# Performance work log

Measured on AMD Instinct MI355X. Metric: run time of the kernel, lower is better.

Reference implementation:

```python
import jax, jax.numpy as jnp
import numpy as np

NOISE_STD = 0.1

def setup_inputs() -> dict:
    key = jax.random.key(0)
    k1, k2, k3, k4 = jax.random.split(key, 4)
    B, S, D, E, NS = 4, 4096, 2048, 64, 10
    x = jax.random.normal(k1, (B, S, D), dtype=jnp.float32)
    W = jax.random.normal(k2, (E, D), dtype=jnp.float32) * (1.0 / np.sqrt(D))
    scale_condition = jax.random.normal(k3, (NS, 1, 1), dtype=jnp.float32)
    noise = jax.random.normal(k4, (B, S, E), dtype=jnp.float32)
    return {"x": x, "W": W, "scale_condition": scale_condition, "noise": noise, "scale_idx": 3}

def reference(x, W, scale_condition, noise, scale_idx):
    TOP_K = 2
    E = W.shape[0]
    # scale modulation: scale_condition[scale_idx] has shape [1,1], broadcasts over [B,S,D]
    scale_factor = scale_condition[scale_idx]
    router_input = x * (1.0 + scale_factor * 0.1)
    # small GEMM: [B,S,D] x [D,E] -> [B,S,E]
    router_logits = jnp.einsum('bsd,ed->bse', router_input, W)
    router_logits = router_logits + noise * NOISE_STD
    routing_probs = jax.nn.softmax(router_logits, axis=-1)
    routing_weights, selected_experts = jax.lax.top_k(routing_probs, TOP_K)
    routing_weights = routing_weights / jnp.sum(routing_weights, axis=-1, keepdims=True)
    # scatter top-k normalized weights into dense [B,S,E] dispatch tensor
    dispatch_tensor = jnp.sum(
        jax.nn.one_hot(selected_experts, E, dtype=routing_weights.dtype)
        * routing_weights[..., None],
        axis=-2,
    )
    return dispatch_tensor, routing_probs, selected_experts
```

## Files before the change

kernel.cpp:

```cpp
#include <hip/hip_runtime.h>
#include <math.h>

#define D        2048
#define E        64
#define NROWS    16384
#define NSLICE   4
#define KSLICE   (D / NSLICE)
#define BK       32
#define TILES    (KSLICE / BK)
#define BM       32
#define XSTR     36
#define OSTR     68
#define PARTIAL_BYTES ((size_t)NSLICE * NROWS * E * 4)

__global__ __launch_bounds__(64)
void gemm_ks(const float* __restrict__ x,
             const float* __restrict__ W,
             const float* __restrict__ scond,
             const int* __restrict__ sidx,
             float* __restrict__ partial)
{
    __shared__ float smem[BM * XSTR + BK * E];
    float* xs = smem;
    float* ws = smem + BM * XSTR;

    const int l = threadIdx.x;
    const int slice   = blockIdx.x & (NSLICE - 1);
    const int rowBase = (blockIdx.x >> 2) * BM;
    const int kBase   = slice * KSLICE;

    const float factor = 1.0f + 0.1f * scond[sidx[0]];

    const int sxr = l >> 1;
    const int sxh = (l & 1) << 4;

    const int rg = l & 7;
    const int eg = l >> 3;

    float acc[4][8];
#pragma unroll
    for (int i = 0; i < 4; ++i)
#pragma unroll
        for (int j = 0; j < 8; ++j) acc[i][j] = 0.f;

    const float* xg = x + (size_t)rowBase * D + kBase;
    const float* wg = W + (size_t)l * D + kBase;

    float4 xb[4], wb[8];
#pragma unroll
    for (int j = 0; j < 4; ++j)
        xb[j] = *(const float4*)(xg + sxr * D + sxh + (j << 2));
#pragma unroll
    for (int j = 0; j < 8; ++j)
        wb[j] = *(const float4*)(wg + (j << 2));

    for (int t = 0; t < TILES; ++t) {
#pragma unroll
        for (int j = 0; j < 4; ++j) {
            float4 v = xb[j];
            v.x *= factor; v.y *= factor; v.z *= factor; v.w *= factor;
            *(float4*)&xs[sxr * XSTR + sxh + (j << 2)] = v;
        }
#pragma unroll
        for (int j = 0; j < 8; ++j) {
            const int k4 = j << 2;
            ws[(k4 + 0) * E + l] = wb[j].x;
            ws[(k4 + 1) * E + l] = wb[j].y;
            ws[(k4 + 2) * E + l] = wb[j].z;
            ws[(k4 + 3) * E + l] = wb[j].w;
        }

        if (t + 1 < TILES) {
            const int k0 = (t + 1) * BK;
#pragma unroll
            for (int j = 0; j < 4; ++j)
                xb[j] = *(const float4*)(xg + sxr * D + k0 + sxh + (j << 2));
#pragma unroll
            for (int j = 0; j < 8; ++j)
                wb[j] = *(const float4*)(wg + k0 + (j << 2));
        }

#pragma unroll
        for (int kc = 0; kc < 8; ++kc) {
            float4 xv[4];
#pragma unroll
            for (int i = 0; i < 4; ++i)
                xv[i] = *(const float4*)&xs[(rg + 8 * i) * XSTR + (kc << 2)];
            float4 wv[8];
#pragma unroll
            for (int k = 0; k < 4; ++k) {
                wv[2 * k]     = *(const float4*)&ws[((kc << 2) + k) * E + (eg << 3)];
                wv[2 * k + 1] = *(const float4*)&ws[((kc << 2) + k) * E + (eg << 3) + 4];
            }
#pragma unroll
            for (int k = 0; k < 4; ++k) {
#pragma unroll
                for (int i = 0; i < 4; ++i) {
                    const float xk = ((const float*)&xv[i])[k];
                    acc[i][0] += xk * wv[2 * k].x;
                    acc[i][1] += xk * wv[2 * k].y;
                    acc[i][2] += xk * wv[2 * k].z;
                    acc[i][3] += xk * wv[2 * k].w;
                    acc[i][4] += xk * wv[2 * k + 1].x;
                    acc[i][5] += xk * wv[2 * k + 1].y;
                    acc[i][6] += xk * wv[2 * k + 1].z;
                    acc[i][7] += xk * wv[2 * k + 1].w;
                }
            }
        }
    }

#pragma unroll
    for (int i = 0; i < 4; ++i) {
        float4 a0, a1;
        a0.x = acc[i][0]; a0.y = acc[i][1]; a0.z = acc[i][2]; a0.w = acc[i][3];
        a1.x = acc[i][4]; a1.y = acc[i][5]; a1.z = acc[i][6]; a1.w = acc[i][7];
        *(float4*)&smem[(rg + 8 * i) * OSTR + (eg << 3)]     = a0;
        *(float4*)&smem[(rg + 8 * i) * OSTR + (eg << 3) + 4] = a1;
    }
    float* pbase = partial + (size_t)slice * NROWS * E + (size_t)rowBase * E;
#pragma unroll
    for (int j = 0; j < 8; ++j) {
        const int p   = (j << 6) + l;
        const int row = p >> 4;
        const int c4  = p & 15;
        const float4 vv = *(const float4*)&smem[row * OSTR + (c4 << 2)];
        *(float4*)(pbase + ((size_t)p << 2)) = vv;
    }
}

__global__ __launch_bounds__(256)
void reduce_topk(const float* __restrict__ partial,
                 const float* __restrict__ noise,
                 float* __restrict__ dispatch,
                 float* __restrict__ probs,
                 float* __restrict__ sel)
{
    const int lane = threadIdx.x & 63;
    const int wave = threadIdx.x >> 6;
    const int row  = blockIdx.x * 4 + wave;

    float v = 0.f;
#pragma unroll
    for (int s = 0; s < NSLICE; ++s)
        v += partial[(size_t)s * NROWS * E + (size_t)row * E + lane];
    v += 0.1f * noise[(size_t)row * E + lane];

    float m = v;
#pragma unroll
    for (int off = 32; off > 0; off >>= 1)
        m = fmaxf(m, __shfl_xor(m, off, 64));
    const float p = expf(v - m);
    float s = p;
#pragma unroll
    for (int off = 32; off > 0; off >>= 1)
        s += __shfl_xor(s, off, 64);
    const float prob = p / s;
    probs[(size_t)row * E + lane] = prob;

    float bv = prob; int bi = lane;
#pragma unroll
    for (int off = 32; off > 0; off >>= 1) {
        const float ov = __shfl_xor(bv, off, 64);
        const int   oi = __shfl_xor(bi, off, 64);
        if (ov > bv || (ov == bv && oi < bi)) { bv = ov; bi = oi; }
    }
    float cv = (lane == bi) ? -INFINITY : prob;
    int ci = lane;
#pragma unroll
    for (int off = 32; off > 0; off >>= 1) {
        const float ov = __shfl_xor(cv, off, 64);
        const int   oi = __shfl_xor(ci, off, 64);
        if (ov > cv || (ov == cv && oi < ci)) { cv = ov; ci = oi; }
    }

    const float sum2 = bv + cv;
    float dval = 0.f;
    if (lane == bi) dval = bv / sum2;
    if (lane == ci) dval = cv / sum2;
    dispatch[(size_t)row * E + lane] = dval;

    if (lane == 0) {
        float2 sv; sv.x = (float)bi; sv.y = (float)ci;
        *(float2*)(sel + (size_t)row * 2) = sv;
    }
}

__global__ __launch_bounds__(256)
void gemm_r2(const float* __restrict__ x, const float* __restrict__ W,
             const float* __restrict__ scond, const float* __restrict__ noise,
             const int* __restrict__ sidx, float* __restrict__ logits_out)
{
    __shared__ float4 xsb[32][17];
    __shared__ float4 wsh[64][16];
    const int tid = threadIdx.x;
    const int rowBase = blockIdx.x * 32;
    const float factor = 1.0f + 0.1f * scond[sidx[0]];
    const int xk = tid & 15, xr = tid >> 4, we = tid & 63, wk = tid >> 6;
    const int eg = tid & 15, rg = tid >> 4, e0 = eg << 2;
    float acc[2][4];
#pragma unroll
    for (int i = 0; i < 2; ++i)
#pragma unroll
        for (int j = 0; j < 4; ++j) acc[i][j] = 0.f;
    const float* xg = x + (size_t)rowBase * D;
    float4 xb[2], wb[4];
#pragma unroll
    for (int i = 0; i < 2; ++i)
        xb[i] = *(const float4*)(xg + (xr + 16 * i) * D + (xk << 2));
#pragma unroll
    for (int j = 0; j < 4; ++j)
        wb[j] = *(const float4*)(W + we * D + (wk << 4) + (j << 2));
    for (int t = 0; t < 32; ++t) {
#pragma unroll
        for (int i = 0; i < 2; ++i) {
            float4 v = xb[i];
            v.x *= factor; v.y *= factor; v.z *= factor; v.w *= factor;
            xsb[xr + 16 * i][xk] = v;
        }
        float* wsf = (float*)wsh;
#pragma unroll
        for (int j = 0; j < 4; ++j) {
            const int kk = (wk << 4) + (j << 2);
            wsf[(kk + 0) * E + we] = wb[j].x;
            wsf[(kk + 1) * E + we] = wb[j].y;
            wsf[(kk + 2) * E + we] = wb[j].z;
            wsf[(kk + 3) * E + we] = wb[j].w;
        }
        __syncthreads();
        if (t + 1 < 32) {
            const int k0 = (t + 1) * 64;
#pragma unroll
            for (int i = 0; i < 2; ++i)
                xb[i] = *(const float4*)(xg + (xr + 16 * i) * D + k0 + (xk << 2));
#pragma unroll
            for (int j = 0; j < 4; ++j)
                wb[j] = *(const float4*)(W + we * D + k0 + (wk << 4) + (j << 2));
        }
#pragma unroll
        for (int kg = 0; kg < 16; ++kg) {
            float4 xv[2], wv[4];
#pragma unroll
            for (int i = 0; i < 2; ++i) xv[i] = xsb[rg + 16 * i][kg];
#pragma unroll
            for (int c = 0; c < 4; ++c) wv[c] = wsh[(kg << 2) + c][eg];
#pragma unroll
            for (int i = 0; i < 2; ++i) {
                const float x0 = xv[i].x, x1 = xv[i].y, x2 = xv[i].z, x3 = xv[i].w;
                acc[i][0] += x0 * wv[0].x; acc[i][1] += x0 * wv[0].y;
                acc[i][2] += x0 * wv[0].z; acc[i][3] += x0 * wv[0].w;
                acc[i][0] += x1 * wv[1].x; acc[i][1] += x1 * wv[1].y;
                acc[i][2] += x1 * wv[1].z; acc[i][3] += x1 * wv[1].w;
                acc[i][0] += x2 * wv[2].x; acc[i][1] += x2 * wv[2].y;
                acc[i][2] += x2 * wv[2].z; acc[i][3] += x2 * wv[2].w;
                acc[i][0] += x3 * wv[3].x; acc[i][1] += x3 * wv[3].y;
                acc[i][2] += x3 * wv[3].z; acc[i][3] += x3 * wv[3].w;
            }
        }
        __syncthreads();
    }
#pragma unroll
    for (int i = 0; i < 2; ++i) {
        const int gRow = rowBase + rg + 16 * i;
        const float4 nz = *(const float4*)(noise + (size_t)gRow * E + e0);
        float4 o;
        o.x = acc[i][0] + 0.1f * nz.x; o.y = acc[i][1] + 0.1f * nz.y;
        o.z = acc[i][2] + 0.1f * nz.z; o.w = acc[i][3] + 0.1f * nz.w;
        *(float4*)(logits_out + (size_t)gRow * E + e0) = o;
    }
}

__global__ __launch_bounds__(256)
void topk_r2(float* __restrict__ probs, float* __restrict__ dispatch,
             float* __restrict__ sel)
{
    const int lane = threadIdx.x & 63;
    const int wave = threadIdx.x >> 6;
    const int row  = blockIdx.x * 4 + wave;
    const float v = probs[(size_t)row * E + lane];
    float m = v;
#pragma unroll
    for (int off = 32; off > 0; off >>= 1)
        m = fmaxf(m, __shfl_xor(m, off, 64));
    const float p = expf(v - m);
    float s = p;
#pragma unroll
    for (int off = 32; off > 0; off >>= 1)
        s += __shfl_xor(s, off, 64);
    const float prob = p / s;
    probs[(size_t)row * E + lane] = prob;
    float bv = prob; int bi = lane;
#pragma unroll
    for (int off = 32; off > 0; off >>= 1) {
        const float ov = __shfl_xor(bv, off, 64);
        const int   oi = __shfl_xor(bi, off, 64);
        if (ov > bv || (ov == bv && oi < bi)) { bv = ov; bi = oi; }
    }
    float cv = (lane == bi) ? -INFINITY : prob;
    int ci = lane;
#pragma unroll
    for (int off = 32; off > 0; off >>= 1) {
        const float ov = __shfl_xor(cv, off, 64);
        const int   oi = __shfl_xor(ci, off, 64);
        if (ov > cv || (ov == cv && oi < ci)) { cv = ov; ci = oi; }
    }
    const float sum2 = bv + cv;
    float dval = 0.f;
    if (lane == bi) dval = bv / sum2;
    if (lane == ci) dval = cv / sum2;
    dispatch[(size_t)row * E + lane] = dval;
    if (lane == 0) {
        float2 sv; sv.x = (float)bi; sv.y = (float)ci;
        *(float2*)(sel + (size_t)row * 2) = sv;
    }
}

extern "C" void kernel_launch(void* const* d_in, const int* in_sizes, int n_in,
                              void* d_out, int out_size, void* d_ws, size_t ws_size,
                              hipStream_t stream) {
    const float* x     = (const float*)d_in[0];
    const float* W     = (const float*)d_in[1];
    const float* scond = (const float*)d_in[2];
    const float* noise = (const float*)d_in[3];
    const int*   sidx  = (const int*)d_in[4];

    float* out      = (float*)d_out;
    float* dispatch = out;
    float* probs    = out + (size_t)NROWS * E;
    float* sel      = out + 2 * (size_t)NROWS * E;

    if (ws_size >= PARTIAL_BYTES) {
        float* partial = (float*)d_ws;
        gemm_ks<<<dim3((NROWS / BM) * NSLICE), dim3(64), 0, stream>>>(
            x, W, scond, sidx, partial);
        reduce_topk<<<dim3(NROWS / 4), dim3(256), 0, stream>>>(
            partial, noise, dispatch, probs, sel);
    } else {
        gemm_r2<<<dim3(NROWS / 32), dim3(256), 0, stream>>>(
            x, W, scond, noise, sidx, probs);
        topk_r2<<<dim3(NROWS / 4), dim3(256), 0, stream>>>(
            probs, dispatch, sel);
    }
}
```

Measured before the change: 225.3 us.

## Use split-fp16 MFMA GEMM fused with softmax/top-k, drop split-K partials

Replaces the FP32 split-K FMA GEMM plus a separate reduce/top-k kernel with a single fused kernel. The GEMM runs on fp16 MFMA instructions, with each operand split into scaled hi/lo halves to emulate FP32 accuracy. A small pre-kernel converts W into hi/lo fp16 buffers in the workspace, and x is converted on the fly into double-buffered LDS. This removes the partial-sum round trip through global memory and uses matrix cores in place of scalar FMAs. In exchange it issues four MFMAs per product and adds conversion work, and accuracy depends on the hi/lo split and the exponent range of fp16.

```diff
diff --git a/kernel.cpp b/kernel.cpp
--- a/kernel.cpp
+++ b/kernel.cpp
@@ -4,185 +4,224 @@
 #define D        2048
 #define E        64
 #define NROWS    16384
-#define NSLICE   4
-#define KSLICE   (D / NSLICE)
-#define BK       32
-#define TILES    (KSLICE / BK)
-#define BM       32
-#define XSTR     36
-#define OSTR     68
-#define PARTIAL_BYTES ((size_t)NSLICE * NROWS * E * 4)
-
-__global__ __launch_bounds__(64)
-void gemm_ks(const float* __restrict__ x,
-             const float* __restrict__ W,
-             const float* __restrict__ scond,
-             const int* __restrict__ sidx,
-             float* __restrict__ partial)
+
+#define ROWS_PB  32
+#define BKC      64
+#define NCH      (D / BKC)
+#define LDX      72
+#define LDW      72
+#define BUF_SHORTS 13824
+#define WCVT_BYTES ((size_t)2 * E * D * sizeof(unsigned short))
+
+#define LSCALE   2048.0f
+#define S1       4.8828125e-4f
+#define S2       2.384185791015625e-7f
+
+typedef __attribute__((ext_vector_type(8))) _Float16 f16x8;
+typedef __attribute__((ext_vector_type(4))) float f32x4;
+
+__device__ __forceinline__ unsigned short f2h(float f) {
+    union { _Float16 h; unsigned short u; } c;
+    c.h = (_Float16)f;
+    return c.u;
+}
+__device__ __forceinline__ float h2f(unsigned short u) {
+    union { _Float16 h; unsigned short u; } c;
+    c.u = u;
+    return (float)c.h;
+}
+
+__global__ __launch_bounds__(256)
+void w_cvt(const float* __restrict__ W,
+           unsigned short* __restrict__ whi,
+           unsigned short* __restrict__ wlo)
 {
-    __shared__ float smem[BM * XSTR + BK * E];
-    float* xs = smem;
-    float* ws = smem + BM * XSTR;
-
-    const int l = threadIdx.x;
-    const int slice   = blockIdx.x & (NSLICE - 1);
-    const int rowBase = (blockIdx.x >> 2) * BM;
-    const int kBase   = slice * KSLICE;
+    const int i = (blockIdx.x * 256 + threadIdx.x) << 3;
+    const float4 a = *(const float4*)(W + i);
+    const float4 b = *(const float4*)(W + i + 4);
+    float vv[8] = {a.x, a.y, a.z, a.w, b.x, b.y, b.z, b.w};
+    unsigned int hw[4], lw[4];
+#pragma unroll
+    for (int j = 0; j < 4; ++j) {
+        const unsigned short h0 = f2h(vv[2*j]);
+        const unsigned short h1 = f2h(vv[2*j+1]);
+        const unsigned short l0 = f2h((vv[2*j]   - h2f(h0)) * LSCALE);
+        const unsigned short l1 = f2h((vv[2*j+1] - h2f(h1)) * LSCALE);
+        hw[j] = (unsigned int)h0 | ((unsigned int)h1 << 16);
+        lw[j] = (unsigned int)l0 | ((unsigned int)l1 << 16);
+    }
+    *(uint4*)(whi + i) = make_uint4(hw[0], hw[1], hw[2], hw[3]);
+    *(uint4*)(wlo + i) = make_uint4(lw[0], lw[1], lw[2], lw[3]);
+}
+
+__global__ __launch_bounds__(256)
+void moe_fused(const float* __restrict__ x,
+               const unsigned short* __restrict__ whi,
+               const unsigned short* __restrict__ wlo,
+               const float* __restrict__ scond,
+               const int* __restrict__ sidx,
+               const float* __restrict__ noise,
+               float* __restrict__ dispatch,
+               float* __restrict__ probs,
+               float* __restrict__ sel)
+{
+    __shared__ unsigned short smem[2 * BUF_SHORTS];
+
+    const int t = threadIdx.x;
+    const int l = t & 63;
+    const int w = t >> 6;
 
     const float factor = 1.0f + 0.1f * scond[sidx[0]];
 
-    const int sxr = l >> 1;
-    const int sxh = (l & 1) << 4;
-
-    const int rg = l & 7;
-    const int eg = l >> 3;
-
-    float acc[4][8];
-#pragma unroll
-    for (int i = 0; i < 4; ++i)
-#pragma unroll
-        for (int j = 0; j < 8; ++j) acc[i][j] = 0.f;
-
-    const float* xg = x + (size_t)rowBase * D + kBase;
-    const float* wg = W + (size_t)l * D + kBase;
-
-    float4 xb[4], wb[8];
-#pragma unroll
-    for (int j = 0; j < 4; ++j)
-        xb[j] = *(const float4*)(xg + sxr * D + sxh + (j << 2));
-#pragma unroll
-    for (int j = 0; j < 8; ++j)
-        wb[j] = *(const float4*)(wg + (j << 2));
-
-    for (int t = 0; t < TILES; ++t) {
-#pragma unroll
-        for (int j = 0; j < 4; ++j) {
-            float4 v = xb[j];
-            v.x *= factor; v.y *= factor; v.z *= factor; v.w *= factor;
-            *(float4*)&xs[sxr * XSTR + sxh + (j << 2)] = v;
-        }
-#pragma unroll
-        for (int j = 0; j < 8; ++j) {
-            const int k4 = j << 2;
-            ws[(k4 + 0) * E + l] = wb[j].x;
-            ws[(k4 + 1) * E + l] = wb[j].y;
-            ws[(k4 + 2) * E + l] = wb[j].z;
-            ws[(k4 + 3) * E + l] = wb[j].w;
-        }
-
-        if (t + 1 < TILES) {
-            const int k0 = (t + 1) * BK;
-#pragma unroll
-            for (int j = 0; j < 4; ++j)
-                xb[j] = *(const float4*)(xg + sxr * D + k0 + sxh + (j << 2));
-#pragma unroll
-            for (int j = 0; j < 8; ++j)
-                wb[j] = *(const float4*)(wg + k0 + (j << 2));
-        }
-
-#pragma unroll
-        for (int kc = 0; kc < 8; ++kc) {
-            float4 xv[4];
-#pragma unroll
-            for (int i = 0; i < 4; ++i)
-                xv[i] = *(const float4*)&xs[(rg + 8 * i) * XSTR + (kc << 2)];
-            float4 wv[8];
-#pragma unroll
-            for (int k = 0; k < 4; ++k) {
-                wv[2 * k]     = *(const float4*)&ws[((kc << 2) + k) * E + (eg << 3)];
-                wv[2 * k + 1] = *(const float4*)&ws[((kc << 2) + k) * E + (eg << 3) + 4];
+    const int xrow = t >> 3;
+    const int xoct = t & 7;
+    const int we_  = t >> 2;
+    const int wko  = (t & 3) << 4;
+
+    const int R  = (w >> 1) << 4;
+    const int CB = (w & 1) << 5;
+    const int fr = l & 15;
+    const int fq = l >> 4;
+
+    const int rowG0 = blockIdx.x * ROWS_PB;
+
+    const float* xg = x + (size_t)(rowG0 + xrow) * D + (xoct << 3);
+    const unsigned short* wgh = whi + (size_t)we_ * D + wko;
+    const unsigned short* wgl = wlo + (size_t)we_ * D + wko;
+
+    f32x4 acc0h = {0.f,0.f,0.f,0.f}, acc0m = {0.f,0.f,0.f,0.f}, acc0l = {0.f,0.f,0.f,0.f};
+    f32x4 acc1h = {0.f,0.f,0.f,0.f}, acc1m = {0.f,0.f,0.f,0.f}, acc1l = {0.f,0.f,0.f,0.f};
+
+    float4 xa = *(const float4*)(xg);
+    float4 xb = *(const float4*)(xg + 4);
+    uint4  wa = *(const uint4*)(wgh);
+    uint4  wb = *(const uint4*)(wgh + 8);
+    uint4  wc = *(const uint4*)(wgl);
+    uint4  wd = *(const uint4*)(wgl + 8);
+
+    for (int c = 0; c < NCH; ++c) {
+        unsigned short* base = smem + (c & 1) * BUF_SHORTS;
+        unsigned short* xh = base;
+        unsigned short* xl = base + 2304;
+        unsigned short* wh = base + 4608;
+        unsigned short* wl = base + 9216;
+
+        {
+            float vv[8] = {xa.x * factor, xa.y * factor, xa.z * factor, xa.w * factor,
+                           xb.x * factor, xb.y * factor, xb.z * factor, xb.w * factor};
+            unsigned int xhw[4], xlw[4];
+#pragma unroll
+            for (int j = 0; j < 4; ++j) {
+                const unsigned short h0 = f2h(vv[2*j]);
+                const unsigned short h1 = f2h(vv[2*j+1]);
+                const unsigned short l0 = f2h((vv[2*j]   - h2f(h0)) * LSCALE);
+                const unsigned short l1 = f2h((vv[2*j+1] - h2f(h1)) * LSCALE);
+                xhw[j] = (unsigned int)h0 | ((unsigned int)h1 << 16);
+                xlw[j] = (unsigned int)l0 | ((unsigned int)l1 << 16);
             }
-#pragma unroll
-            for (int k = 0; k < 4; ++k) {
-#pragma unroll
-                for (int i = 0; i < 4; ++i) {
-                    const float xk = ((const float*)&xv[i])[k];
-                    acc[i][0] += xk * wv[2 * k].x;
-                    acc[i][1] += xk * wv[2 * k].y;
-                    acc[i][2] += xk * wv[2 * k].z;
-                    acc[i][3] += xk * wv[2 * k].w;
-                    acc[i][4] += xk * wv[2 * k + 1].x;
-                    acc[i][5] += xk * wv[2 * k + 1].y;
-                    acc[i][6] += xk * wv[2 * k + 1].z;
-                    acc[i][7] += xk * wv[2 * k + 1].w;
-                }
-            }
-        }
-    }
-
-#pragma unroll
-    for (int i = 0; i < 4; ++i) {
-        float4 a0, a1;
-        a0.x = acc[i][0]; a0.y = acc[i][1]; a0.z = acc[i][2]; a0.w = acc[i][3];
-        a1.x = acc[i][4]; a1.y = acc[i][5]; a1.z = acc[i][6]; a1.w = acc[i][7];
-        *(float4*)&smem[(rg + 8 * i) * OSTR + (eg << 3)]     = a0;
-        *(float4*)&smem[(rg + 8 * i) * OSTR + (eg << 3) + 4] = a1;
-    }
-    float* pbase = partial + (size_t)slice * NROWS * E + (size_t)rowBase * E;
-#pragma unroll
-    for (int j = 0; j < 8; ++j) {
-        const int p   = (j << 6) + l;
-        const int row = p >> 4;
-        const int c4  = p & 15;
-        const float4 vv = *(const float4*)&smem[row * OSTR + (c4 << 2)];
-        *(float4*)(pbase + ((size_t)p << 2)) = vv;
-    }
-}
-
-__global__ __launch_bounds__(256)
-void reduce_topk(const float* __restrict__ partial,
-                 const float* __restrict__ noise,
-                 float* __restrict__ dispatch,
-                 float* __restrict__ probs,
-                 float* __restrict__ sel)
-{
-    const int lane = threadIdx.x & 63;
-    const int wave = threadIdx.x >> 6;
-    const int row  = blockIdx.x * 4 + wave;
-
-    float v = 0.f;
-#pragma unroll
-    for (int s = 0; s < NSLICE; ++s)
-        v += partial[(size_t)s * NROWS * E + (size_t)row * E + lane];
-    v += 0.1f * noise[(size_t)row * E + lane];
-
-    float m = v;
-#pragma unroll
-    for (int off = 32; off > 0; off >>= 1)
-        m = fmaxf(m, __shfl_xor(m, off, 64));
-    const float p = expf(v - m);
-    float s = p;
-#pragma unroll
-    for (int off = 32; off > 0; off >>= 1)
-        s += __shfl_xor(s, off, 64);
-    const float prob = p / s;
-    probs[(size_t)row * E + lane] = prob;
-
-    float bv = prob; int bi = lane;
-#pragma unroll
-    for (int off = 32; off > 0; off >>= 1) {
-        const float ov = __shfl_xor(bv, off, 64);
-        const int   oi = __shfl_xor(bi, off, 64);
-        if (ov > bv || (ov == bv && oi < bi)) { bv = ov; bi = oi; }
-    }
-    float cv = (lane == bi) ? -INFINITY : prob;
-    int ci = lane;
-#pragma unroll
-    for (int off = 32; off > 0; off >>= 1) {
-        const float ov = __shfl_xor(cv, off, 64);
-        const int   oi = __shfl_xor(ci, off, 64);
-        if (ov > cv || (ov == cv && oi < ci)) { cv = ov; ci = oi; }
-    }
-
-    const float sum2 = bv + cv;
-    float dval = 0.f;
-    if (lane == bi) dval = bv / sum2;
-    if (lane == ci) dval = cv / sum2;
-    dispatch[(size_t)row * E + lane] = dval;
-
-    if (lane == 0) {
-        float2 sv; sv.x = (float)bi; sv.y = (float)ci;
-        *(float2*)(sel + (size_t)row * 2) = sv;
+            const int o = xrow * LDX + (xoct << 3);
+            *(uint4*)&xh[o] = make_uint4(xhw[0], xhw[1], xhw[2], xhw[3]);
+            *(uint4*)&xl[o] = make_uint4(xlw[0], xlw[1], xlw[2], xlw[3]);
+        }
+        {
+            const int o = we_ * LDW + wko;
+            *(uint4*)&wh[o]     = wa;
+            *(uint4*)&wh[o + 8] = wb;
+            *(uint4*)&wl[o]     = wc;
+            *(uint4*)&wl[o + 8] = wd;
+        }
+
+        __syncthreads();
+
+        if (c + 1 < NCH) {
+            const int k0 = (c + 1) << 6;
+            xa = *(const float4*)(xg + k0);
+            xb = *(const float4*)(xg + k0 + 4);
+            wa = *(const uint4*)(wgh + k0);
+            wb = *(const uint4*)(wgh + k0 + 8);
+            wc = *(const uint4*)(wgl + k0);
+            wd = *(const uint4*)(wgl + k0 + 8);
+        }
+
+#pragma unroll
+        for (int ks = 0; ks < 2; ++ks) {
+            const int ko = (ks << 5) + (fq << 3);
+            const f16x8 ah  = *(const f16x8*)&xh[(R + fr) * LDX + ko];
+            const f16x8 al  = *(const f16x8*)&xl[(R + fr) * LDX + ko];
+            const f16x8 b0h = *(const f16x8*)&wh[(CB + fr) * LDW + ko];
+            const f16x8 b0l = *(const f16x8*)&wl[(CB + fr) * LDW + ko];
+            const f16x8 b1h = *(const f16x8*)&wh[(CB + 16 + fr) * LDW + ko];
+            const f16x8 b1l = *(const f16x8*)&wl[(CB + 16 + fr) * LDW + ko];
+            acc0h = __builtin_amdgcn_mfma_f32_16x16x32_f16(ah, b0h, acc0h, 0, 0, 0);
+            acc0m = __builtin_amdgcn_mfma_f32_16x16x32_f16(ah, b0l, acc0m, 0, 0, 0);
+            acc0m = __builtin_amdgcn_mfma_f32_16x16x32_f16(al, b0h, acc0m, 0, 0, 0);
+            acc0l = __builtin_amdgcn_mfma_f32_16x16x32_f16(al, b0l, acc0l, 0, 0, 0);
+            acc1h = __builtin_amdgcn_mfma_f32_16x16x32_f16(ah, b1h, acc1h, 0, 0, 0);
+            acc1m = __builtin_amdgcn_mfma_f32_16x16x32_f16(ah, b1l, acc1m, 0, 0, 0);
+            acc1m = __builtin_amdgcn_mfma_f32_16x16x32_f16(al, b1h, acc1m, 0, 0, 0);
+            acc1l = __builtin_amdgcn_mfma_f32_16x16x32_f16(al, b1l, acc1l, 0, 0, 0);
+        }
+    }
+
+    __syncthreads();
+    float* lg = (float*)smem;
+#pragma unroll
+    for (int j = 0; j < 4; ++j) {
+        const int rr = R + (fq << 2) + j;
+        lg[rr * 68 + CB + fr]      = acc0h[j] + S1 * acc0m[j] + S2 * acc0l[j];
+        lg[rr * 68 + CB + 16 + fr] = acc1h[j] + S1 * acc1m[j] + S2 * acc1l[j];
+    }
+    __syncthreads();
+
+    const int r0 = w << 3;
+    float nz[8];
+#pragma unroll
+    for (int i = 0; i < 8; ++i)
+        nz[i] = noise[(size_t)(rowG0 + r0 + i) * E + l];
+
+#pragma unroll 2
+    for (int i = 0; i < 8; ++i) {
+        const int G = rowG0 + r0 + i;
+        const float v = lg[(r0 + i) * 68 + l] + 0.1f * nz[i];
+
+        float m = v;
+#pragma unroll
+        for (int off = 32; off > 0; off >>= 1)
+            m = fmaxf(m, __shfl_xor(m, off, 64));
+        const float p = expf(v - m);
+        float s = p;
+#pragma unroll
+        for (int off = 32; off > 0; off >>= 1)
+            s += __shfl_xor(s, off, 64);
+        const float prob = p / s;
+        probs[(size_t)G * E + l] = prob;
+
+        float bv = prob; int bi = l;
+#pragma unroll
+        for (int off = 32; off > 0; off >>= 1) {
+            const float ov = __shfl_xor(bv, off, 64);
+            const int   oi = __shfl_xor(bi, off, 64);
+            if (ov > bv || (ov == bv && oi < bi)) { bv = ov; bi = oi; }
+        }
+        float cv = (l == bi) ? -INFINITY : prob;
+        int ci = l;
+#pragma unroll
+        for (int off = 32; off > 0; off >>= 1) {
+            const float ov = __shfl_xor(cv, off, 64);
+            const int   oi = __shfl_xor(ci, off, 64);
+            if (ov > cv || (ov == cv && oi < ci)) { cv = ov; ci = oi; }
+        }
+
+        const float sum2 = bv + cv;
+        float dval = 0.f;
+        if (l == bi) dval = bv / sum2;
+        if (l == ci) dval = cv / sum2;
+        dispatch[(size_t)G * E + l] = dval;
+
+        if (l == 0) {
+            float2 sv; sv.x = (float)bi; sv.y = (float)ci;
+            *(float2*)(sel + (size_t)G * 2) = sv;
+        }
     }
 }
 
@@ -329,12 +368,12 @@
     float* probs    = out + (size_t)NROWS * E;
     float* sel      = out + 2 * (size_t)NROWS * E;
 
-    if (ws_size >= PARTIAL_BYTES) {
-        float* partial = (float*)d_ws;
-        gemm_ks<<<dim3((NROWS / BM) * NSLICE), dim3(64), 0, stream>>>(
-            x, W, scond, sidx, partial);
-        reduce_topk<<<dim3(NROWS / 4), dim3(256), 0, stream>>>(
-            partial, noise, dispatch, probs, sel);
+    if (ws_size >= WCVT_BYTES) {
+        unsigned short* whi = (unsigned short*)d_ws;
+        unsigned short* wlo = whi + (size_t)E * D;
+        w_cvt<<<dim3(64), dim3(256), 0, stream>>>(W, whi, wlo);
+        moe_fused<<<dim3(NROWS / ROWS_PB), dim3(256), 0, stream>>>(
+            x, whi, wlo, scond, sidx, noise, dispatch, probs, sel);
     } else {
         gemm_r2<<<dim3(NROWS / 32), dim3(256), 0, stream>>>(
             x, W, scond, noise, sidx, probs);
```

Measured after the change: 223.7 us. Within noise of the previous version (-0.7%).
